# Performance work log

Hardware: AMD Instinct MI355X
Metric: run time of the kernel (lower is better)

Reference implementation:

```python
import jax, jax.numpy as jnp
import numpy as np

B, T, N, FIN = 32, 12, 1024, 64
K, OUT_F = 3, 64


def setup_inputs() -> dict:
    key = jax.random.key(0)
    k1, k2, k3 = jax.random.split(key, 3)
    x = jax.random.normal(k1, (B, T, N, FIN), dtype=jnp.float32)
    A = jax.random.uniform(k2, (B, N, N), dtype=jnp.float32)
    # Xavier-uniform-like init for Theta [K, in_f, out_f]
    limit = float(np.sqrt(6.0 / (FIN + OUT_F)))
    Theta = jax.random.uniform(k3, (K, FIN, OUT_F), dtype=jnp.float32,
                               minval=-limit, maxval=limit)
    return {"x": x, "A": A, "Theta": Theta}


def reference(x, A, Theta):
    Bb, Tt, Nn, Fin = x.shape
    Kk = Theta.shape[0]
    I = jnp.broadcast_to(jnp.eye(Nn, dtype=x.dtype), (Bb, Nn, Nn))
    # lambda_max = max row-sum of A, clamped to >= 1
    lambda_max = jnp.maximum(jnp.max(jnp.sum(A, axis=-1), axis=-1), 1.0)
    L = 2.0 * A / lambda_max[:, None, None] - I  # scaled Laplacian surrogate [B,N,N]
    out = jnp.zeros((Bb, Tt, Nn, Theta.shape[-1]), dtype=x.dtype)
    T_prev2, T_prev = None, I
    for k in range(Kk):  # small fixed K-hop loop
        if k == 0:
            T_k = I
        elif k == 1:
            T_k = L
        else:
            T_k = 2.0 * jnp.einsum('bnm,bmp->bnp', L, T_prev) - T_prev2
        T_prev2, T_prev = T_prev, T_k
        rhs = jnp.einsum('btnf,fo->btno', x, Theta[k])   # feature transform
        out = out + jnp.einsum('bnm,btmo->btno', T_k, rhs)  # graph aggregation
    return jax.nn.relu(out)
```

## Files before the change

kernel.cpp:

```cpp
#include <hip/hip_runtime.h>

typedef unsigned short ushort_t;
typedef unsigned char uchar_t;
typedef __attribute__((ext_vector_type(8))) __bf16 bf16x8;
typedef __attribute__((ext_vector_type(4))) float f32x4;
typedef __attribute__((ext_vector_type(8))) unsigned short u16x8;
typedef __attribute__((ext_vector_type(8))) int i32x8;

#define NB 32
#define TT 12
#define NNODE 1024
#define FF 64
#define OO 64
#define TO 768

#define SCL_ONE 127
#define SCL_E   118

__device__ __forceinline__ unsigned short f2bf(float f) {
    unsigned u = __float_as_uint(f);
    u += 0x7FFFu + ((u >> 16) & 1u);
    return (unsigned short)(u >> 16);
}
__device__ __forceinline__ float bf2f(unsigned short h) {
    return __uint_as_float(((unsigned)h) << 16);
}
__device__ __forceinline__ unsigned char f2fp8(float f) {
    return (unsigned char)(__builtin_amdgcn_cvt_pk_fp8_f32(f, f, 0, false) & 0xff);
}

__device__ __forceinline__ void gload16(const void* g, void* l) {
    __builtin_amdgcn_global_load_lds(
        (const __attribute__((address_space(1))) unsigned int*)g,
        (__attribute__((address_space(3))) unsigned int*)l, 16, 0, 0);
}

__global__ void k_init(unsigned* lam) {
    if (threadIdx.x < NB) lam[threadIdx.x] = 0x3F800000u;
}

__global__ __launch_bounds__(256) void k_rowmax(const float* __restrict__ A,
                                                unsigned* __restrict__ lam) {
    const int b = blockIdx.x >> 4;
    const int chunk = blockIdx.x & 15;
    const int w = threadIdx.x >> 6, lane = threadIdx.x & 63;
    const float* Ab = A + (size_t)b * NNODE * NNODE;
    float mx = 0.0f;
    for (int r = 0; r < 16; ++r) {
        const float* rp = Ab + (size_t)(chunk * 64 + w * 16 + r) * NNODE;
        float s = 0.0f;
#pragma unroll
        for (int j = 0; j < 16; ++j) s += rp[lane + j * 64];
#pragma unroll
        for (int off = 32; off > 0; off >>= 1) s += __shfl_down(s, off, 64);
        if (lane == 0) mx = fmaxf(mx, s);
    }
    if (lane == 0) atomicMax(&lam[b], __float_as_uint(mx));
}

__global__ __launch_bounds__(256) void k_escale(const float* __restrict__ A,
                                                const unsigned* __restrict__ lam,
                                                uchar_t* __restrict__ E8) {
    const size_t idx = ((size_t)blockIdx.x * 256 + threadIdx.x) * 8;
    const int b = (int)(idx >> 20);
    const float scl = 1024.0f / __uint_as_float(lam[b]);
    const float4 v0 = *(const float4*)(A + idx);
    const float4 v1 = *(const float4*)(A + idx + 4);
    unsigned lo = 0, hi = 0;
    lo = (unsigned)__builtin_amdgcn_cvt_pk_fp8_f32(v0.x * scl, v0.y * scl, (int)lo, false);
    lo = (unsigned)__builtin_amdgcn_cvt_pk_fp8_f32(v0.z * scl, v0.w * scl, (int)lo, true);
    hi = (unsigned)__builtin_amdgcn_cvt_pk_fp8_f32(v1.x * scl, v1.y * scl, (int)hi, false);
    hi = (unsigned)__builtin_amdgcn_cvt_pk_fp8_f32(v1.z * scl, v1.w * scl, (int)hi, true);
    uint2 pk; pk.x = lo; pk.y = hi;
    *(uint2*)(E8 + idx) = pk;
}

__global__ void k_theta(const float* __restrict__ Th, ushort_t* __restrict__ Tht) {
    int tid = blockIdx.x * 256 + threadIdx.x;
    if (tid < 3 * 64 * 64) {
        int k = tid >> 12, rem = tid & 4095, o = rem >> 6, f = rem & 63;
        Tht[tid] = f2bf(Th[(k << 12) + (f << 6) + o]);
    }
}

__global__ __launch_bounds__(512, 5) void k_feature(const float* __restrict__ x,
                                                    const ushort_t* __restrict__ Tht,
                                                    ushort_t* __restrict__ Pb,
                                                    ushort_t* __restrict__ Qc,
                                                    uchar_t* __restrict__ R2f8) {
    __shared__ __align__(16) uchar_t th[3 * 64 * 128];
    __shared__ __align__(16) uchar_t tbuf[26624];
    ushort_t* tbq = (ushort_t*)tbuf;
    char* tbr = (char*)(tbuf + 17408);

    const int n0 = blockIdx.x * 128;
    const int t = blockIdx.y;
    const int b = blockIdx.z;
    const int tid = threadIdx.x;
    const int w = tid >> 6, lane = tid & 63, quad = lane >> 4, l15 = lane & 15;

#pragma unroll
    for (int i = 0; i < 3; ++i) {
        int chunk = i * 512 + tid;
        int ko = chunk >> 3, c = chunk & 7;
        int phys = c ^ (ko & 7);
        const int4 v = *(const int4*)(Tht + ko * 64 + c * 8);
        *(int4*)(th + ko * 128 + phys * 16) = v;
    }

    const float* xr = x + (((size_t)b * TT + t) * NNODE + n0 + w * 16 + l15) * FF;
    bf16x8 af[2];
#pragma unroll
    for (int ks = 0; ks < 2; ++ks) {
        const float4 v0 = *(const float4*)(xr + ks * 32 + quad * 8);
        const float4 v1 = *(const float4*)(xr + ks * 32 + quad * 8 + 4);
        u16x8 p;
        p[0] = f2bf(v0.x); p[1] = f2bf(v0.y); p[2] = f2bf(v0.z); p[3] = f2bf(v0.w);
        p[4] = f2bf(v1.x); p[5] = f2bf(v1.y); p[6] = f2bf(v1.z); p[7] = f2bf(v1.w);
        af[ks] = *(bf16x8*)&p;
    }
    __syncthreads();

    f32x4 acc[3][4];
#pragma unroll
    for (int k = 0; k < 3; ++k)
#pragma unroll
        for (int cb = 0; cb < 4; ++cb) acc[k][cb] = (f32x4){0.f, 0.f, 0.f, 0.f};

#pragma unroll
    for (int k = 0; k < 3; ++k)
#pragma unroll
        for (int ks = 0; ks < 2; ++ks)
#pragma unroll
            for (int cb = 0; cb < 4; ++cb) {
                const int o = cb * 16 + l15;
                const int c = (ks * 4 + quad) ^ (o & 7);
                const bf16x8 bfr = *(const bf16x8*)(th + (k * 64 + o) * 128 + c * 16);
                acc[k][cb] = __builtin_amdgcn_mfma_f32_16x16x32_bf16(af[ks], bfr, acc[k][cb], 0, 0, 0);
            }

    ushort_t* Pbb = Pb + (((size_t)b * TT + t) * NNODE + n0) * OO;
#pragma unroll
    for (int cb = 0; cb < 4; ++cb)
#pragma unroll
        for (int r = 0; r < 4; ++r) {
            const int n = w * 16 + quad * 4 + r;
            const int o = cb * 16 + l15;
            Pbb[(size_t)n * OO + o] = f2bf(acc[0][cb][r] - acc[2][cb][r]);
        }

#pragma unroll
    for (int cb = 0; cb < 4; ++cb)
#pragma unroll
        for (int r = 0; r < 4; ++r) {
            const int nl = w * 16 + quad * 4 + r;
            const int o = cb * 16 + l15;
            tbq[o * 136 + nl] = f2bf(acc[1][cb][r] - 2.0f * acc[2][cb][r]);
            tbr[o * 144 + nl] = (char)f2fp8(acc[2][cb][r]);
        }
    __syncthreads();

    {
        const int o = tid >> 3, seg = tid & 7;
        ushort_t* qrow = Qc + ((size_t)b * TO + t * 64 + o) * NNODE + n0 + seg * 16;
        const ushort_t* sq = tbq + o * 136 + seg * 16;
        *(u16x8*)(qrow) = *(const u16x8*)(sq);
        *(u16x8*)(qrow + 8) = *(const u16x8*)(sq + 8);
        uchar_t* rrow = R2f8 + ((size_t)b * TO + t * 64 + o) * NNODE + n0 + seg * 16;
        *(int4*)rrow = *(const int4*)(tbr + o * 144 + seg * 16);
    }
}

template <int MODE>
__global__ __launch_bounds__(256) void k_gemm8(const uchar_t* __restrict__ Aop, size_t aBS,
                                               const uchar_t* __restrict__ Bop, size_t bBS,
                                               const ushort_t* __restrict__ Qc,
                                               uchar_t* __restrict__ Zf8,
                                               ushort_t* __restrict__ Pbp,
                                               float* __restrict__ outp) {
    __shared__ __align__(16) uchar_t smem[34816];
    uchar_t* At = smem;
    uchar_t* Bt = smem + 16384;
    const int bid = blockIdx.x;
    const int xcd = bid & 7, y = bid >> 3;
    const int tile = y % 48;
    const int b = xcd + 8 * (y / 48);
    const int tm = (MODE == 1) ? (tile >> 3) : (tile / 6);
    const int tn = (MODE == 1) ? (tile & 7) : (tile % 6);
    const int m0 = tm * 128, n0 = tn * 128;
    const int tid = threadIdx.x;
    const int w = tid >> 6, lane = tid & 63, quad = lane >> 4, l15 = lane & 15;
    const int wr = w >> 1, wc = w & 1;
    const uchar_t* Ab = Aop + (size_t)b * aBS + (size_t)m0 * NNODE;
    const uchar_t* Bb = Bop + (size_t)b * bBS + (size_t)n0 * NNODE;

    int ldso[4];
    size_t goff[4];
#pragma unroll
    for (int i = 0; i < 4; ++i) {
        int slot = i * 256 + tid;
        int row = slot >> 3;
        int lc = (slot & 7) ^ (row & 7);
        ldso[i] = slot * 16;
        goff[i] = (size_t)row * NNODE + lc * 16;
    }

    f32x4 acc[4][4];
#pragma unroll
    for (int i = 0; i < 4; ++i)
#pragma unroll
        for (int j = 0; j < 4; ++j) acc[i][j] = (f32x4){0.f, 0.f, 0.f, 0.f};

    for (int kk = 0; kk < 8; ++kk) {
        const int k0 = kk << 7;
#pragma unroll
        for (int i = 0; i < 4; ++i) {
            gload16(Ab + k0 + goff[i], At + ldso[i]);
            gload16(Bb + k0 + goff[i], Bt + ldso[i]);
        }
        __syncthreads();
        i32x8 af[4], bfr[4];
#pragma unroll
        for (int i = 0; i < 4; ++i) {
            const int m = wr * 64 + i * 16 + l15;
            const int n = wc * 64 + i * 16 + l15;
            const int4 alo = *(const int4*)(At + m * 128 + (((quad << 1)) ^ (m & 7)) * 16);
            const int4 ahi = *(const int4*)(At + m * 128 + (((quad << 1) | 1) ^ (m & 7)) * 16);
            const int4 blo = *(const int4*)(Bt + n * 128 + (((quad << 1)) ^ (n & 7)) * 16);
            const int4 bhi = *(const int4*)(Bt + n * 128 + (((quad << 1) | 1) ^ (n & 7)) * 16);
            af[i] = (i32x8){alo.x, alo.y, alo.z, alo.w, ahi.x, ahi.y, ahi.z, ahi.w};
            bfr[i] = (i32x8){blo.x, blo.y, blo.z, blo.w, bhi.x, bhi.y, bhi.z, bhi.w};
        }
#pragma unroll
        for (int i = 0; i < 4; ++i)
#pragma unroll
            for (int j = 0; j < 4; ++j)
                acc[i][j] = __builtin_amdgcn_mfma_scale_f32_16x16x128_f8f6f4(
                    af[i], bfr[j], acc[i][j], 0, 0, 0, SCL_ONE, 0, SCL_E);
        __syncthreads();
    }

    if (MODE == 1) {
        ushort_t* tb = (ushort_t*)smem;
        const ushort_t* Qb = Qc + (size_t)b * TO * NNODE;
        uchar_t* Zb = Zf8 + (size_t)b * TO * NNODE;
#pragma unroll
        for (int i = 0; i < 4; ++i)
#pragma unroll
            for (int r = 0; r < 4; ++r) {
                const int cl = wr * 64 + i * 16 + quad * 4 + r;
                const int c = m0 + cl;
#pragma unroll
                for (int j = 0; j < 4; ++j) {
                    const int nl = wc * 64 + j * 16 + l15;
                    const size_t zi = (size_t)c * NNODE + n0 + nl;
                    const float z = bf2f(Qb[zi]) + 2.0f * acc[i][j][r];
                    Zb[zi] = f2fp8(z);
                    tb[nl * 136 + cl] = f2bf(z);
                }
            }
        __syncthreads();
        const int t0 = m0 >> 6;
        const int row = tid >> 1, half = tid & 1;
        ushort_t* prow = Pbp + (((size_t)b * TT + t0 + half) * NNODE + n0 + row) * OO;
        const ushort_t* srow = tb + row * 136 + half * 64;
#pragma unroll
        for (int s = 0; s < 8; ++s) {
            u16x8 pv = *(const u16x8*)(prow + s * 8);
            u16x8 zv = *(const u16x8*)(srow + s * 8);
            u16x8 rv;
#pragma unroll
            for (int e = 0; e < 8; ++e) rv[e] = f2bf(bf2f(pv[e]) - bf2f(zv[e]));
            *(u16x8*)(prow + s * 8) = rv;
        }
    } else {
#pragma unroll
        for (int i = 0; i < 4; ++i)
#pragma unroll
            for (int r = 0; r < 4; ++r) {
                const int n = m0 + wr * 64 + i * 16 + quad * 4 + r;
#pragma unroll
                for (int j = 0; j < 4; ++j) {
                    const int c = n0 + wc * 64 + j * 16 + l15;
                    const int t = c >> 6, o = c & 63;
                    const size_t id = (((size_t)b * TT + t) * NNODE + n) * OO + o;
                    outp[id] = fmaxf(bf2f(Pbp[id]) + acc[i][j][r], 0.0f);
                }
            }
    }
}

extern "C" void kernel_launch(void* const* d_in, const int* in_sizes, int n_in,
                              void* d_out, int out_size, void* d_ws, size_t ws_size,
                              hipStream_t stream) {
    const float* x = (const float*)d_in[0];
    const float* A = (const float*)d_in[1];
    const float* Th = (const float*)d_in[2];
    float* out = (float*)d_out;
    char* ws = (char*)d_ws;

    unsigned* lam = (unsigned*)ws;
    uchar_t* E8 = (uchar_t*)(ws + 256);
    uchar_t* R2f8 = E8 + (size_t)NB * NNODE * NNODE;
    uchar_t* Zf8 = R2f8 + (size_t)NB * TO * NNODE;
    ushort_t* Qc = (ushort_t*)(Zf8 + (size_t)NB * TO * NNODE);
    ushort_t* Pb = Qc + (size_t)NB * TO * NNODE;
    ushort_t* Tht = Pb + (size_t)NB * TT * NNODE * OO;

    k_init<<<1, 64, 0, stream>>>(lam);
    k_rowmax<<<512, 256, 0, stream>>>(A, lam);
    k_escale<<<16384, 256, 0, stream>>>(A, lam, E8);
    k_theta<<<48, 256, 0, stream>>>(Th, Tht);
    k_feature<<<dim3(8, 12, 32), 512, 0, stream>>>(x, Tht, Pb, Qc, R2f8);
    k_gemm8<1><<<1536, 256, 0, stream>>>(R2f8, (size_t)TO * NNODE,
                                         E8, (size_t)NNODE * NNODE,
                                         Qc, Zf8, Pb, nullptr);
    k_gemm8<2><<<1536, 256, 0, stream>>>(E8, (size_t)NNODE * NNODE,
                                         Zf8, (size_t)TO * NNODE,
                                         nullptr, nullptr, Pb, out);
}
```

Measured before the change: 465.6 us.

## Vectorize rowmax, swizzle epilogue LDS, stagger K order, raise GEMM occupancy

The row-sum kernel now reads A with float4 loads instead of scalar loads. The fp8 GEMM shrinks its LDS footprint from 34816 to 32768 bytes by replacing the padded transpose buffer with an XOR-swizzled layout, and it requests a minimum of 5 blocks per SM through launch_bounds. Each block also starts its K loop at a different phase, so concurrent blocks read different K slices of the shared batch operands, spreading cache and channel traffic. The risks are register spilling from the tighter launch bound and possible bank conflicts in the new swizzle pattern.

```diff
diff --git a/kernel.cpp b/kernel.cpp
--- a/kernel.cpp
+++ b/kernel.cpp
@@ -47,10 +47,14 @@
     const float* Ab = A + (size_t)b * NNODE * NNODE;
     float mx = 0.0f;
     for (int r = 0; r < 16; ++r) {
-        const float* rp = Ab + (size_t)(chunk * 64 + w * 16 + r) * NNODE;
-        float s = 0.0f;
-#pragma unroll
-        for (int j = 0; j < 16; ++j) s += rp[lane + j * 64];
+        const float4* rp = (const float4*)(Ab + (size_t)(chunk * 64 + w * 16 + r) * NNODE);
+        float4 s4 = {0.f, 0.f, 0.f, 0.f};
+#pragma unroll
+        for (int p = 0; p < 4; ++p) {
+            const float4 v = rp[p * 64 + lane];
+            s4.x += v.x; s4.y += v.y; s4.z += v.z; s4.w += v.w;
+        }
+        float s = (s4.x + s4.y) + (s4.z + s4.w);
 #pragma unroll
         for (int off = 32; off > 0; off >>= 1) s += __shfl_down(s, off, 64);
         if (lane == 0) mx = fmaxf(mx, s);
@@ -172,13 +176,13 @@
 }
 
 template <int MODE>
-__global__ __launch_bounds__(256) void k_gemm8(const uchar_t* __restrict__ Aop, size_t aBS,
-                                               const uchar_t* __restrict__ Bop, size_t bBS,
-                                               const ushort_t* __restrict__ Qc,
-                                               uchar_t* __restrict__ Zf8,
-                                               ushort_t* __restrict__ Pbp,
-                                               float* __restrict__ outp) {
-    __shared__ __align__(16) uchar_t smem[34816];
+__global__ __launch_bounds__(256, 5) void k_gemm8(const uchar_t* __restrict__ Aop, size_t aBS,
+                                                  const uchar_t* __restrict__ Bop, size_t bBS,
+                                                  const ushort_t* __restrict__ Qc,
+                                                  uchar_t* __restrict__ Zf8,
+                                                  ushort_t* __restrict__ Pbp,
+                                                  float* __restrict__ outp) {
+    __shared__ __align__(16) uchar_t smem[32768];
     uchar_t* At = smem;
     uchar_t* Bt = smem + 16384;
     const int bid = blockIdx.x;
@@ -191,6 +195,7 @@
     const int tid = threadIdx.x;
     const int w = tid >> 6, lane = tid & 63, quad = lane >> 4, l15 = lane & 15;
     const int wr = w >> 1, wc = w & 1;
+    const int phase = y & 7;
     const uchar_t* Ab = Aop + (size_t)b * aBS + (size_t)m0 * NNODE;
     const uchar_t* Bb = Bop + (size_t)b * bBS + (size_t)n0 * NNODE;
 
@@ -211,7 +216,8 @@
 #pragma unroll
         for (int j = 0; j < 4; ++j) acc[i][j] = (f32x4){0.f, 0.f, 0.f, 0.f};
 
-    for (int kk = 0; kk < 8; ++kk) {
+    for (int it = 0; it < 8; ++it) {
+        const int kk = (it + phase) & 7;
         const int k0 = kk << 7;
 #pragma unroll
         for (int i = 0; i < 4; ++i) {
@@ -256,22 +262,23 @@
                     const size_t zi = (size_t)c * NNODE + n0 + nl;
                     const float z = bf2f(Qb[zi]) + 2.0f * acc[i][j][r];
                     Zb[zi] = f2fp8(z);
-                    tb[nl * 136 + cl] = f2bf(z);
+                    tb[nl * 128 + (((cl >> 3) ^ (nl & 15)) << 3) + (cl & 7)] = f2bf(z);
                 }
             }
         __syncthreads();
         const int t0 = m0 >> 6;
-        const int row = tid >> 1, half = tid & 1;
-        ushort_t* prow = Pbp + (((size_t)b * TT + t0 + half) * NNODE + n0 + row) * OO;
-        const ushort_t* srow = tb + row * 136 + half * 64;
-#pragma unroll
-        for (int s = 0; s < 8; ++s) {
-            u16x8 pv = *(const u16x8*)(prow + s * 8);
-            u16x8 zv = *(const u16x8*)(srow + s * 8);
+        const int row = tid >> 1, seg = tid & 1;
+        ushort_t* prow = Pbp + (((size_t)b * TT + t0 + seg) * NNODE + n0 + row) * OO;
+#pragma unroll
+        for (int k = 0; k < 8; ++k) {
+            const int ch = seg * 8 + k;
+            const ushort_t* src = tb + row * 128 + ((ch ^ (row & 15)) << 3);
+            u16x8 pv = *(const u16x8*)(prow + k * 8);
+            u16x8 zv = *(const u16x8*)src;
             u16x8 rv;
 #pragma unroll
             for (int e = 0; e < 8; ++e) rv[e] = f2bf(bf2f(pv[e]) - bf2f(zv[e]));
-            *(u16x8*)(prow + s * 8) = rv;
+            *(u16x8*)(prow + k * 8) = rv;
         }
     } else {
 #pragma unroll
```

Result: slower. 796.4 us (+71.1%).
